# Kernel optimization log

Hardware: AMD Instinct MI355X
Metric: run time of the kernel (lower is better)

## Reference

```python
import jax, jax.numpy as jnp
import numpy as np

DIM = 2048
NUM_HEADS = 16
HEAD_DIM = DIM // NUM_HEADS  # 128


def setup_inputs() -> dict:
    key = jax.random.key(0)
    ks = jax.random.split(key, 5)
    scale = 0.02
    x = jax.random.normal(ks[0], (1, 2048, DIM), dtype=jnp.float32)
    # nn.Linear weights stored as [out_features, in_features]
    Wq = jax.random.normal(ks[1], (DIM, DIM), dtype=jnp.float32) * scale
    Wk = jax.random.normal(ks[2], (HEAD_DIM, DIM), dtype=jnp.float32) * scale
    Wv = jax.random.normal(ks[3], (HEAD_DIM, DIM), dtype=jnp.float32) * scale
    Wo = jax.random.normal(ks[4], (DIM, DIM), dtype=jnp.float32) * scale
    return {"x": x, "Wq": Wq, "Wk": Wk, "Wv": Wv, "Wo": Wo}


def reference(x, Wq, Wk, Wv, Wo):
    batch, seq_len, dim = x.shape
    q = x @ Wq.T                                   # [b, s, dim]
    k = x @ Wk.T                                   # [b, s, head_dim] (shared across heads)
    v = x @ Wv.T                                   # [b, s, head_dim]
    q = q.reshape(batch, seq_len, NUM_HEADS, HEAD_DIM).transpose(0, 2, 1, 3)  # [b, h, s, d]
    # MQA: single KV head broadcast across query heads (no materialized repeat)
    scores = jnp.einsum("bhqd,bkd->bhqk", q, k) / (HEAD_DIM ** 0.5)
    probs = jax.nn.softmax(scores, axis=-1)        # [b, h, q, k]
    out = jnp.einsum("bhqk,bkd->bhqd", probs, v)   # [b, h, s, d]
    out = out.transpose(0, 2, 1, 3).reshape(batch, seq_len, dim)
    return out @ Wo.T
```

## Files before the change

### kernel.cpp

```cpp
#include <hip/hip_runtime.h>
#include <cmath>

typedef float  float4_t __attribute__((ext_vector_type(4)));
typedef __bf16 bf16x8   __attribute__((ext_vector_type(8)));
typedef unsigned short u16;

__device__ __forceinline__ u16 f2bf(float f) {
    unsigned u = __float_as_uint(f);
    u += 0x7fffu + ((u >> 16) & 1u);
    return (u16)(u >> 16);
}
__device__ __forceinline__ u16 f2bf_hu(float f) {
    return (u16)((__float_as_uint(f) + 0x8000u) >> 16);
}

#define GLOAD_LDS16(g, l)                                              \
    __builtin_amdgcn_global_load_lds(                                  \
        (__attribute__((address_space(1))) void*)(g),                  \
        (__attribute__((address_space(3))) void*)(l), 16, 0, 0)

__global__ __launch_bounds__(256) void cast_all(const float* __restrict__ x,
                                                const float* __restrict__ wq,
                                                const float* __restrict__ wk,
                                                const float* __restrict__ wv,
                                                const float* __restrict__ wo,
                                                u16* __restrict__ xb, u16* __restrict__ wqb,
                                                u16* __restrict__ wkb, u16* __restrict__ wvb,
                                                u16* __restrict__ wob) {
    const int b = blockIdx.x;
    const float* src;
    u16* dst;
    int i;
    if (b < 4096)      { src = x;  dst = xb;  i = b * 256 + threadIdx.x; }
    else if (b < 8192) { src = wq; dst = wqb; i = (b - 4096) * 256 + threadIdx.x; }
    else if (b < 8448) { src = wk; dst = wkb; i = (b - 8192) * 256 + threadIdx.x; }
    else if (b < 8704) { src = wv; dst = wvb; i = (b - 8448) * 256 + threadIdx.x; }
    else               { src = wo; dst = wob; i = (b - 8704) * 256 + threadIdx.x; }
    float4 f = ((const float4*)src)[i];
    ushort4 r;
    r.x = f2bf(f.x); r.y = f2bf(f.y); r.z = f2bf(f.z); r.w = f2bf(f.w);
    ((ushort4*)dst)[i] = r;
}

template <typename EPI>
__device__ __forceinline__ void gemm_core(const u16* __restrict__ A,
                                          const u16* __restrict__ B,
                                          int K, int bm, int bn, EPI epi) {
    __shared__ __align__(16) u16 As[2 * 64 * 32];
    __shared__ __align__(16) u16 Bs[2 * 128 * 32];
    const int tid  = threadIdx.x;
    const int lane = tid & 63, wave = tid >> 6;
    const int quad = lane >> 4, l16 = lane & 15;

    float4_t acc[4][2] = {};

    for (int k0 = 0; k0 < K; k0 += 64) {
#pragma unroll
        for (int i = 0; i < 2; ++i) {
            const int slot = i * 256 + tid;
            const int ks = slot >> 8, win = slot & 255;
            const int row = win >> 2, ch = (win & 3) * 8;
            GLOAD_LDS16(A + (size_t)(bm + row) * K + k0 + ks * 32 + ch, &As[slot * 8]);
        }
#pragma unroll
        for (int i = 0; i < 4; ++i) {
            const int slot = i * 256 + tid;
            const int ks = slot >> 9, win = slot & 511;
            const int row = win >> 2, ch = (win & 3) * 8;
            GLOAD_LDS16(B + (size_t)(bn + row) * K + k0 + ks * 32 + ch, &Bs[slot * 8]);
        }
        __syncthreads();

        bf16x8 af[2][4], bfr[2][2];
#pragma unroll
        for (int ks = 0; ks < 2; ++ks) {
#pragma unroll
            for (int mi = 0; mi < 4; ++mi)
                af[ks][mi] = *(const bf16x8*)&As[ks * 2048 + (mi * 16 + l16) * 32 + quad * 8];
#pragma unroll
            for (int ni = 0; ni < 2; ++ni)
                bfr[ks][ni] = *(const bf16x8*)&Bs[ks * 4096 + (wave * 32 + ni * 16 + l16) * 32 + quad * 8];
        }
#pragma unroll
        for (int mi = 0; mi < 4; ++mi)
#pragma unroll
            for (int ni = 0; ni < 2; ++ni) {
                acc[mi][ni] = __builtin_amdgcn_mfma_f32_16x16x32_bf16(
                    af[0][mi], bfr[0][ni], acc[mi][ni], 0, 0, 0);
                acc[mi][ni] = __builtin_amdgcn_mfma_f32_16x16x32_bf16(
                    af[1][mi], bfr[1][ni], acc[mi][ni], 0, 0, 0);
            }
        __syncthreads();
    }

#pragma unroll
    for (int mi = 0; mi < 4; ++mi) {
        const int row = bm + mi * 16 + quad * 4;
#pragma unroll
        for (int ni = 0; ni < 2; ++ni) {
            const int col = bn + wave * 32 + ni * 16 + l16;
#pragma unroll
            for (int r = 0; r < 4; ++r) epi(row + r, col, acc[mi][ni][r]);
        }
    }
}

__global__ __launch_bounds__(256) void gemm_qkv(const u16* __restrict__ A,
                                                const u16* __restrict__ B,
                                                u16* __restrict__ qb,
                                                u16* __restrict__ kb,
                                                u16* __restrict__ vtb) {
    gemm_core(A, B, 2048, blockIdx.x * 64, blockIdx.y * 128,
              [=](int row, int col, float v) {
                  if (col < 2048)
                      qb[(size_t)row * 2048 + col] = f2bf(v * 0.1275174313451427f);
                  else if (col < 2176)
                      kb[(size_t)row * 128 + (col - 2048)] = f2bf(v);
                  else
                      vtb[(size_t)(col - 2176) * 2048 + row] = f2bf(v);
              });
}

__global__ __launch_bounds__(256) void gemm_out(const u16* __restrict__ A,
                                                const u16* __restrict__ B,
                                                float* __restrict__ C) {
    gemm_core(A, B, 2048, blockIdx.x * 64, blockIdx.y * 128,
              [=](int row, int col, float v) {
                  C[(size_t)row * 2048 + col] = v;
              });
}

__global__ __launch_bounds__(256) void mqa_attn(const u16* __restrict__ Q,
                                                const u16* __restrict__ Kmat,
                                                const u16* __restrict__ Vt,
                                                float* __restrict__ Oacc0,
                                                float* __restrict__ Oacc1,
                                                float* __restrict__ Lsum) {
    __shared__ __align__(16) u16 Ks[4 * 32 * 32];
    __shared__ __align__(16) u16 Vts[128 * 32];
    __shared__ __align__(16) u16 Ps[4][32 * 40];
    const int tid  = threadIdx.x;
    const int wave = tid >> 6, lane = tid & 63;
    const int quad = lane >> 4, l16 = lane & 15;
    const int h     = blockIdx.y;
    const int ks    = blockIdx.z;
    const int qbase = blockIdx.x * 128 + wave * 32;
    const int kbase = ks * 1024;

    bf16x8 qf[2][4];
#pragma unroll
    for (int mt = 0; mt < 2; ++mt)
#pragma unroll
        for (int kb4 = 0; kb4 < 4; ++kb4)
            qf[mt][kb4] = *(const bf16x8*)(Q + (size_t)(qbase + mt * 16 + l16) * 2048 +
                                           h * 128 + kb4 * 32 + quad * 8);

    float4_t acc[2][8];
#pragma unroll
    for (int mt = 0; mt < 2; ++mt)
#pragma unroll
        for (int nt = 0; nt < 8; ++nt) acc[mt][nt] = (float4_t){0.f, 0.f, 0.f, 0.f};
    float lsum[8] = {};

    bf16x8 pa_prev[2];
    bf16x8 vf_prev[8];

    u16* pb = Ps[wave];

    for (int s = 0; s < 32; ++s) {
        const int k0 = kbase + s * 32;
#pragma unroll
        for (int i = 0; i < 2; ++i) {
            const int slot = i * 256 + tid;
            const int kb4 = slot >> 7, win = slot & 127;
            const int row = win >> 2, ch = (win & 3) * 8;
            GLOAD_LDS16(Kmat + (size_t)(k0 + row) * 128 + kb4 * 32 + ch, &Ks[slot * 8]);
        }
#pragma unroll
        for (int i = 0; i < 2; ++i) {
            const int slot = i * 256 + tid;
            const int d = slot >> 2, ch = (slot & 3) * 8;
            GLOAD_LDS16(Vt + (size_t)d * 2048 + k0 + ch, &Vts[slot * 8]);
        }
        __syncthreads();

        if (s > 0) {
#pragma unroll
            for (int nt = 0; nt < 8; ++nt) {
                acc[0][nt] = __builtin_amdgcn_mfma_f32_16x16x32_bf16(pa_prev[0], vf_prev[nt], acc[0][nt], 0, 0, 0);
                acc[1][nt] = __builtin_amdgcn_mfma_f32_16x16x32_bf16(pa_prev[1], vf_prev[nt], acc[1][nt], 0, 0, 0);
            }
        }

#pragma unroll
        for (int ct = 0; ct < 2; ++ct) {
            float4_t s0 = (float4_t){0.f, 0.f, 0.f, 0.f};
            float4_t s1 = (float4_t){0.f, 0.f, 0.f, 0.f};
#pragma unroll
            for (int kb4 = 0; kb4 < 4; ++kb4) {
                bf16x8 kf = *(const bf16x8*)&Ks[kb4 * 1024 + (ct * 16 + l16) * 32 + quad * 8];
                s0 = __builtin_amdgcn_mfma_f32_16x16x32_bf16(qf[0][kb4], kf, s0, 0, 0, 0);
                s1 = __builtin_amdgcn_mfma_f32_16x16x32_bf16(qf[1][kb4], kf, s1, 0, 0, 0);
            }
#pragma unroll
            for (int r = 0; r < 4; ++r) {
                const float e0 = exp2f(s0[r]);
                const float e1 = exp2f(s1[r]);
                lsum[r]     += e0;
                lsum[4 + r] += e1;
                pb[(quad * 4 + r) * 40 + ct * 16 + l16]      = f2bf_hu(e0);
                pb[(16 + quad * 4 + r) * 40 + ct * 16 + l16] = f2bf_hu(e1);
            }
        }
#pragma unroll
        for (int mt = 0; mt < 2; ++mt)
            pa_prev[mt] = *(const bf16x8*)&pb[(mt * 16 + l16) * 40 + quad * 8];
#pragma unroll
        for (int nt = 0; nt < 8; ++nt)
            vf_prev[nt] = *(const bf16x8*)&Vts[(nt * 16 + l16) * 32 + quad * 8];
        __syncthreads();
    }

#pragma unroll
    for (int nt = 0; nt < 8; ++nt) {
        acc[0][nt] = __builtin_amdgcn_mfma_f32_16x16x32_bf16(pa_prev[0], vf_prev[nt], acc[0][nt], 0, 0, 0);
        acc[1][nt] = __builtin_amdgcn_mfma_f32_16x16x32_bf16(pa_prev[1], vf_prev[nt], acc[1][nt], 0, 0, 0);
    }

    float* __restrict__ Op = ks ? Oacc1 : Oacc0;
#pragma unroll
    for (int mt = 0; mt < 2; ++mt)
#pragma unroll
        for (int r = 0; r < 4; ++r) {
            const int row = qbase + mt * 16 + quad * 4 + r;
            const size_t base = ((size_t)h * 2048 + row) * 128;
            float lrow = lsum[mt * 4 + r];
#pragma unroll
            for (int off = 1; off < 16; off <<= 1) lrow += __shfl_xor(lrow, off);
            if (l16 == 0) Lsum[(size_t)ks * 32768 + h * 2048 + row] = lrow;
#pragma unroll
            for (int nt = 0; nt < 8; ++nt)
                Op[base + nt * 16 + l16] = acc[mt][nt][r];
        }
}

__global__ __launch_bounds__(256) void attn_combine(const float* __restrict__ O0,
                                                    const float* __restrict__ O1,
                                                    const float* __restrict__ L,
                                                    u16* __restrict__ attn) {
    const int f = blockIdx.x * 256 + threadIdx.x;
    const int d4 = f & 31, h = (f >> 5) & 15, q = f >> 9;
    const int li = h * 2048 + q;
    const float inv = 1.0f / (L[li] + L[32768 + li]);
    const int oi = li * 32 + d4;
    const float4 a = ((const float4*)O0)[oi];
    const float4 b = ((const float4*)O1)[oi];
    ushort4 r;
    r.x = f2bf((a.x + b.x) * inv);
    r.y = f2bf((a.y + b.y) * inv);
    r.z = f2bf((a.z + b.z) * inv);
    r.w = f2bf((a.w + b.w) * inv);
    ((ushort4*)attn)[f] = r;
}

extern "C" void kernel_launch(void* const* d_in, const int* in_sizes, int n_in,
                              void* d_out, int out_size, void* d_ws, size_t ws_size,
                              hipStream_t stream) {
    const float* x  = (const float*)d_in[0];
    const float* Wq = (const float*)d_in[1];
    const float* Wk = (const float*)d_in[2];
    const float* Wv = (const float*)d_in[3];
    const float* Wo = (const float*)d_in[4];
    float* out = (float*)d_out;

    u16* ws   = (u16*)d_ws;
    u16* xb   = ws;
    u16* Wqb  = xb  + (4 << 20);
    u16* Wkb  = Wqb + (4 << 20);
    u16* Wvb  = Wkb + (256 << 10);
    u16* Wob  = Wvb + (256 << 10);
    u16* qb   = Wob + (4 << 20);
    u16* kb   = qb  + (4 << 20);
    u16* vtb  = kb  + (256 << 10);
    u16* attn = vtb + (256 << 10);
    float* Oacc0 = (float*)ws;
    float* Oacc1 = (float*)(attn + (4 << 20));
    float* Lsum  = Oacc1 + (4 << 20);

    cast_all<<<12800, 256, 0, stream>>>(x, Wq, Wk, Wv, Wo, xb, Wqb, Wkb, Wvb, Wob);

    gemm_qkv<<<dim3(32, 18), 256, 0, stream>>>(xb, Wqb, qb, kb, vtb);
    mqa_attn<<<dim3(16, 16, 2), 256, 0, stream>>>(qb, kb, vtb, Oacc0, Oacc1, Lsum);
    attn_combine<<<4096, 256, 0, stream>>>(Oacc0, Oacc1, Lsum, attn);
    gemm_out<<<dim3(32, 16), 256, 0, stream>>>(attn, Wob, out);
}
```

Before: 233.3 us.

## Swizzle LDS tiles in GEMM and attention, widen attention key tile to 64

Adds an XOR-free rotation swizzle to the global->LDS load addresses and the matching LDS fragment reads in both the GEMM core and the MQA attention kernel, to cut LDS bank conflicts on the 32-element rows. The attention loop now handles 64 keys per iteration instead of 32, halving the number of barriers and loads per key. It also drops the deferred software-pipelined PV MFMA, so PV is computed right after softmax in the same iteration. The wider tile raises LDS use and register pressure, and losing the pipelining may expose latency.

```diff
diff --git a/kernel.cpp b/kernel.cpp
--- a/kernel.cpp
+++ b/kernel.cpp
@@ -18,6 +18,9 @@
     __builtin_amdgcn_global_load_lds(                                  \
         (__attribute__((address_space(1))) void*)(g),                  \
         (__attribute__((address_space(3))) void*)(l), 16, 0, 0)
+
+__device__ __forceinline__ int sw_st(int cs, int row) { return ((cs - (row >> 1)) & 3) * 8; }
+__device__ __forceinline__ int sw_rd(int quad, int row) { return (((quad + (row >> 1)) & 3)) * 8; }
 
 __global__ __launch_bounds__(256) void cast_all(const float* __restrict__ x,
                                                 const float* __restrict__ wq,
@@ -59,15 +62,17 @@
         for (int i = 0; i < 2; ++i) {
             const int slot = i * 256 + tid;
             const int ks = slot >> 8, win = slot & 255;
-            const int row = win >> 2, ch = (win & 3) * 8;
-            GLOAD_LDS16(A + (size_t)(bm + row) * K + k0 + ks * 32 + ch, &As[slot * 8]);
+            const int row = win >> 2;
+            GLOAD_LDS16(A + (size_t)(bm + row) * K + k0 + ks * 32 + sw_st(win & 3, row),
+                        &As[slot * 8]);
         }
 #pragma unroll
         for (int i = 0; i < 4; ++i) {
             const int slot = i * 256 + tid;
             const int ks = slot >> 9, win = slot & 511;
-            const int row = win >> 2, ch = (win & 3) * 8;
-            GLOAD_LDS16(B + (size_t)(bn + row) * K + k0 + ks * 32 + ch, &Bs[slot * 8]);
+            const int row = win >> 2;
+            GLOAD_LDS16(B + (size_t)(bn + row) * K + k0 + ks * 32 + sw_st(win & 3, row),
+                        &Bs[slot * 8]);
         }
         __syncthreads();
 
@@ -75,11 +80,15 @@
 #pragma unroll
         for (int ks = 0; ks < 2; ++ks) {
 #pragma unroll
-            for (int mi = 0; mi < 4; ++mi)
-                af[ks][mi] = *(const bf16x8*)&As[ks * 2048 + (mi * 16 + l16) * 32 + quad * 8];
-#pragma unroll
-            for (int ni = 0; ni < 2; ++ni)
-                bfr[ks][ni] = *(const bf16x8*)&Bs[ks * 4096 + (wave * 32 + ni * 16 + l16) * 32 + quad * 8];
+            for (int mi = 0; mi < 4; ++mi) {
+                const int rw = mi * 16 + l16;
+                af[ks][mi] = *(const bf16x8*)&As[ks * 2048 + rw * 32 + sw_rd(quad, rw)];
+            }
+#pragma unroll
+            for (int ni = 0; ni < 2; ++ni) {
+                const int rw = wave * 32 + ni * 16 + l16;
+                bfr[ks][ni] = *(const bf16x8*)&Bs[ks * 4096 + rw * 32 + sw_rd(quad, rw)];
+            }
         }
 #pragma unroll
         for (int mi = 0; mi < 4; ++mi)
@@ -136,9 +145,9 @@
                                                 float* __restrict__ Oacc0,
                                                 float* __restrict__ Oacc1,
                                                 float* __restrict__ Lsum) {
-    __shared__ __align__(16) u16 Ks[4 * 32 * 32];
-    __shared__ __align__(16) u16 Vts[128 * 32];
-    __shared__ __align__(16) u16 Ps[4][32 * 40];
+    __shared__ __align__(16) u16 Ks[4 * 64 * 32];
+    __shared__ __align__(16) u16 Vts[2 * 128 * 32];
+    __shared__ __align__(16) u16 Ps[4][32 * 72];
     const int tid  = threadIdx.x;
     const int wave = tid >> 6, lane = tid & 63;
     const int quad = lane >> 4, l16 = lane & 15;
@@ -162,43 +171,36 @@
         for (int nt = 0; nt < 8; ++nt) acc[mt][nt] = (float4_t){0.f, 0.f, 0.f, 0.f};
     float lsum[8] = {};
 
-    bf16x8 pa_prev[2];
-    bf16x8 vf_prev[8];
-
     u16* pb = Ps[wave];
 
-    for (int s = 0; s < 32; ++s) {
-        const int k0 = kbase + s * 32;
-#pragma unroll
-        for (int i = 0; i < 2; ++i) {
+    for (int s = 0; s < 16; ++s) {
+        const int k0 = kbase + s * 64;
+#pragma unroll
+        for (int i = 0; i < 4; ++i) {
             const int slot = i * 256 + tid;
-            const int kb4 = slot >> 7, win = slot & 127;
-            const int row = win >> 2, ch = (win & 3) * 8;
-            GLOAD_LDS16(Kmat + (size_t)(k0 + row) * 128 + kb4 * 32 + ch, &Ks[slot * 8]);
-        }
-#pragma unroll
-        for (int i = 0; i < 2; ++i) {
+            const int kb4 = slot >> 8, win = slot & 255;
+            const int row = win >> 2;
+            GLOAD_LDS16(Kmat + (size_t)(k0 + row) * 128 + kb4 * 32 + sw_st(win & 3, row),
+                        &Ks[slot * 8]);
+        }
+#pragma unroll
+        for (int i = 0; i < 4; ++i) {
             const int slot = i * 256 + tid;
-            const int d = slot >> 2, ch = (slot & 3) * 8;
-            GLOAD_LDS16(Vt + (size_t)d * 2048 + k0 + ch, &Vts[slot * 8]);
+            const int kk = slot >> 9, win = slot & 511;
+            const int row = win >> 2;
+            GLOAD_LDS16(Vt + (size_t)row * 2048 + k0 + kk * 32 + sw_st(win & 3, row),
+                        &Vts[slot * 8]);
         }
         __syncthreads();
 
-        if (s > 0) {
-#pragma unroll
-            for (int nt = 0; nt < 8; ++nt) {
-                acc[0][nt] = __builtin_amdgcn_mfma_f32_16x16x32_bf16(pa_prev[0], vf_prev[nt], acc[0][nt], 0, 0, 0);
-                acc[1][nt] = __builtin_amdgcn_mfma_f32_16x16x32_bf16(pa_prev[1], vf_prev[nt], acc[1][nt], 0, 0, 0);
-            }
-        }
-
-#pragma unroll
-        for (int ct = 0; ct < 2; ++ct) {
+#pragma unroll
+        for (int ct = 0; ct < 4; ++ct) {
             float4_t s0 = (float4_t){0.f, 0.f, 0.f, 0.f};
             float4_t s1 = (float4_t){0.f, 0.f, 0.f, 0.f};
 #pragma unroll
             for (int kb4 = 0; kb4 < 4; ++kb4) {
-                bf16x8 kf = *(const bf16x8*)&Ks[kb4 * 1024 + (ct * 16 + l16) * 32 + quad * 8];
+                const int rw = ct * 16 + l16;
+                bf16x8 kf = *(const bf16x8*)&Ks[kb4 * 2048 + rw * 32 + sw_rd(quad, rw)];
                 s0 = __builtin_amdgcn_mfma_f32_16x16x32_bf16(qf[0][kb4], kf, s0, 0, 0, 0);
                 s1 = __builtin_amdgcn_mfma_f32_16x16x32_bf16(qf[1][kb4], kf, s1, 0, 0, 0);
             }
@@ -208,23 +210,26 @@
                 const float e1 = exp2f(s1[r]);
                 lsum[r]     += e0;
                 lsum[4 + r] += e1;
-                pb[(quad * 4 + r) * 40 + ct * 16 + l16]      = f2bf_hu(e0);
-                pb[(16 + quad * 4 + r) * 40 + ct * 16 + l16] = f2bf_hu(e1);
-            }
-        }
+                pb[(quad * 4 + r) * 72 + ct * 16 + l16]      = f2bf_hu(e0);
+                pb[(16 + quad * 4 + r) * 72 + ct * 16 + l16] = f2bf_hu(e1);
+            }
+        }
+        bf16x8 pa[2][2];
 #pragma unroll
         for (int mt = 0; mt < 2; ++mt)
-            pa_prev[mt] = *(const bf16x8*)&pb[(mt * 16 + l16) * 40 + quad * 8];
-#pragma unroll
-        for (int nt = 0; nt < 8; ++nt)
-            vf_prev[nt] = *(const bf16x8*)&Vts[(nt * 16 + l16) * 32 + quad * 8];
+#pragma unroll
+            for (int kk = 0; kk < 2; ++kk)
+                pa[mt][kk] = *(const bf16x8*)&pb[(mt * 16 + l16) * 72 + kk * 32 + quad * 8];
+#pragma unroll
+        for (int kk = 0; kk < 2; ++kk)
+#pragma unroll
+            for (int nt = 0; nt < 8; ++nt) {
+                const int rw = nt * 16 + l16;
+                bf16x8 vf = *(const bf16x8*)&Vts[kk * 4096 + rw * 32 + sw_rd(quad, rw)];
+                acc[0][nt] = __builtin_amdgcn_mfma_f32_16x16x32_bf16(pa[0][kk], vf, acc[0][nt], 0, 0, 0);
+                acc[1][nt] = __builtin_amdgcn_mfma_f32_16x16x32_bf16(pa[1][kk], vf, acc[1][nt], 0, 0, 0);
+            }
         __syncthreads();
-    }
-
-#pragma unroll
-    for (int nt = 0; nt < 8; ++nt) {
-        acc[0][nt] = __builtin_amdgcn_mfma_f32_16x16x32_bf16(pa_prev[0], vf_prev[nt], acc[0][nt], 0, 0, 0);
-        acc[1][nt] = __builtin_amdgcn_mfma_f32_16x16x32_bf16(pa_prev[1], vf_prev[nt], acc[1][nt], 0, 0, 0);
     }
 
     float* __restrict__ Op = ks ? Oacc1 : Oacc0;
```

After: 226.7 us. 1.03x faster.
